# Kernel tuning notes

Measured on AMD Instinct MI355X. Metric: run time of the kernel, lower is better.

## Reference

```python
import jax, jax.numpy as jnp
import numpy as np

V = 32000; D = 256; H = 8; L = 2; FF = 1024; S = 512; B = 32
M = 4096          # mem_max_entries
NC = 10           # num_classes
K = 4             # retrieve top-k
TH = 0.5          # write threshold
EPS = 1e-8


def setup_inputs() -> dict:
    key = jax.random.key(0)
    ks = jax.random.split(key, 24)
    s = 0.02
    def nrm(k, shape):
        return jax.random.normal(k, shape, jnp.float32) * s
    return {
        "input_ids": jax.random.randint(ks[0], (B, S), 0, V),
        "tok_emb": nrm(ks[1], (V, D)),
        "pos_emb": nrm(ks[2], (S, D)),
        # per-layer params stacked on leading dim L
        "Wqkv": nrm(ks[3], (L, 3 * D, D)), "bqkv": jnp.zeros((L, 3 * D)),
        "Wo": nrm(ks[4], (L, D, D)), "bo": jnp.zeros((L, D)),
        "ln1_g": jnp.ones((L, D)), "ln1_b": jnp.zeros((L, D)),
        "W1": nrm(ks[5], (L, FF, D)), "b1": jnp.zeros((L, FF)),
        "W2": nrm(ks[6], (L, D, FF)), "b2": jnp.zeros((L, D)),
        "ln2_g": jnp.ones((L, D)), "ln2_b": jnp.zeros((L, D)),
        # write gate MLP (d -> d -> 1, sigmoid)
        "Wg1": nrm(ks[7], (D, D)), "bg1": jnp.zeros((D,)),
        "Wg2": nrm(ks[8], (1, D)), "bg2": jnp.zeros((1,)),
        # classifier
        "Wc": nrm(ks[9], (NC, D)), "bc": jnp.zeros((NC,)),
    }


def _layer_norm(x, g, b):
    m = x.mean(-1, keepdims=True)
    v = ((x - m) ** 2).mean(-1, keepdims=True)
    return (x - m) / jnp.sqrt(v + 1e-5) * g + b


def _encoder_layer(x, Wqkv, bqkv, Wo, bo, g1, b1, W1, bf1, W2, bf2, g2, b2):
    # post-LN TransformerEncoderLayer, relu activation, batch_first
    Bx, Sx, Dx = x.shape
    dh = Dx // H
    qkv = x @ Wqkv.T + bqkv                     # [B,S,3D]
    q, k, v = jnp.split(qkv, 3, axis=-1)
    def heads(t):
        return t.reshape(Bx, Sx, H, dh).transpose(0, 2, 1, 3)  # [B,H,S,dh]
    q, k, v = heads(q), heads(k), heads(v)
    scores = jnp.einsum("bhqd,bhkd->bhqk", q, k) / jnp.sqrt(jnp.float32(dh))
    attn = jax.nn.softmax(scores, axis=-1)
    o = jnp.einsum("bhqk,bhkd->bhqd", attn, v)
    o = o.transpose(0, 2, 1, 3).reshape(Bx, Sx, Dx)
    o = o @ Wo.T + bo
    x = _layer_norm(x + o, g1, b1)
    ff = jax.nn.relu(x @ W1.T + bf1) @ W2.T + bf2
    return _layer_norm(x + ff, g2, b2)


def reference(input_ids, tok_emb, pos_emb, Wqkv, bqkv, Wo, bo, ln1_g, ln1_b,
              W1, b1, W2, b2, ln2_g, ln2_b, Wg1, bg1, Wg2, bg2, Wc, bc):
    Bx, Sx = input_ids.shape
    x = tok_emb[input_ids] + pos_emb[jnp.arange(Sx)][None, :, :]
    for l in range(L):
        x = _encoder_layer(x, Wqkv[l], bqkv[l], Wo[l], bo[l], ln1_g[l], ln1_b[l],
                           W1[l], b1[l], W2[l], b2[l], ln2_g[l], ln2_b[l])
    h = x                                        # [B,S,D]
    cls_state = h[:, 0, :]                       # [B,D]

    # --- write gate: per-token store into external memory (capped FIFO scatter) ---
    flat_h = h.reshape(-1, D)                    # [B*S, D]
    probs = jax.nn.sigmoid(jax.nn.relu(flat_h @ Wg1.T + bg1) @ Wg2.T + bg2)[:, 0]
    mask = probs > TH                            # [B*S]
    slot = jnp.cumsum(mask.astype(jnp.int32)) - 1
    valid = mask & (slot < M)
    idx = jnp.where(valid, slot, M)              # overflow -> dummy row M
    mem = jnp.zeros((M + 1, D), jnp.float32).at[idx].set(flat_h)[:M]
    count = jnp.minimum(mask.sum(), M)
    occupied = jnp.arange(M) < count             # [M]

    # --- top-k cosine retrieval with CLS as query ---
    qn = cls_state / (jnp.linalg.norm(cls_state, axis=-1, keepdims=True) + EPS)
    kn = mem / (jnp.linalg.norm(mem, axis=-1, keepdims=True) + EPS)
    sims = qn @ kn.T                             # [B,M]
    sims = jnp.where(occupied[None, :], sims, -1e9)
    top_sims, top_idx = jax.lax.top_k(sims, K)   # [B,K]
    vals = mem[top_idx]                          # [B,K,D] (unoccupied rows are zero)
    attn = jax.nn.softmax(top_sims, axis=-1)
    mem_vec = jnp.einsum("bk,bkd->bd", attn, vals)
    mem_vec = jnp.where(count > 0, mem_vec, 0.0)

    cls_aug = cls_state + mem_vec
    return cls_aug @ Wc.T + bc                   # [B,NC]
```

## Files before the change

kernel.cpp:

```cpp
#include <hip/hip_runtime.h>
#include <math.h>

#define D_   256
#define H_   8
#define L_   2
#define FF_  1024
#define S_   512
#define B_   32
#define M_   4096
#define NC_  10
#define ROWS (B_*S_)

typedef __attribute__((ext_vector_type(8))) short bf16x8;
typedef __attribute__((ext_vector_type(4))) float f32x4;
typedef unsigned int uint32;

__device__ __forceinline__ float wave_sum(float v) {
#pragma unroll
  for (int off = 1; off < 64; off <<= 1) v += __shfl_xor(v, off, 64);
  return v;
}

__device__ __forceinline__ unsigned short bf16_rne(float x) {
  unsigned int b = __float_as_uint(x);
  return (unsigned short)((b + 0x7FFFu + ((b >> 16) & 1u)) >> 16);
}
__device__ __forceinline__ float bf16_f(unsigned short h) {
  return __uint_as_float(((unsigned int)h) << 16);
}
__device__ __forceinline__ uint32 pack_split(float x) {
  const unsigned short h = bf16_rne(x);
  const unsigned short l = bf16_rne(x - bf16_f(h));
  return (uint32)h | ((uint32)l << 16);
}
__device__ __forceinline__ void unpack_store(unsigned short* Hq, unsigned short* Lq,
                                             int off, uint4 v) {
  uint2 hp, lp;
  hp.x = (v.x & 0xffffu) | (v.y << 16);
  hp.y = (v.z & 0xffffu) | (v.w << 16);
  lp.x = (v.x >> 16) | (v.y & 0xffff0000u);
  lp.y = (v.z >> 16) | (v.w & 0xffff0000u);
  *(uint2*)&Hq[off] = hp;
  *(uint2*)&Lq[off] = lp;
}
__device__ __forceinline__ bf16x8 ld_frag(const unsigned short* p, int off) {
  union { uint2 u[2]; bf16x8 v; } x;
  x.u[0] = *(const uint2*)(p + off);
  x.u[1] = *(const uint2*)(p + off + 4);
  return x.v;
}

__global__ __launch_bounds__(256) void pack_f32(const float* __restrict__ src,
                                                uint32* __restrict__ dst, int n4) {
  const int i = blockIdx.x * 256 + threadIdx.x;
  if (i < n4) {
    const float4 v = ((const float4*)src)[i];
    uint4 o;
    o.x = pack_split(v.x); o.y = pack_split(v.y);
    o.z = pack_split(v.z); o.w = pack_split(v.w);
    ((uint4*)dst)[i] = o;
  }
}

__global__ __launch_bounds__(256) void emb_kernel(const int* __restrict__ ids,
                                                  const float* __restrict__ tok,
                                                  const float* __restrict__ pos,
                                                  float* __restrict__ x,
                                                  uint32* __restrict__ xp) {
  const int row  = blockIdx.x * 4 + (threadIdx.x >> 6);
  const int lane = threadIdx.x & 63;
  const int id = ids[row];
  const int s  = row & (S_ - 1);
  const float4 t = *(const float4*)(tok + (size_t)id * D_ + lane * 4);
  const float4 p = *(const float4*)(pos + (size_t)s  * D_ + lane * 4);
  float4 r; r.x = t.x + p.x; r.y = t.y + p.y; r.z = t.z + p.z; r.w = t.w + p.w;
  *(float4*)(x + (size_t)row * D_ + lane * 4) = r;
  uint4 o;
  o.x = pack_split(r.x); o.y = pack_split(r.y);
  o.z = pack_split(r.z); o.w = pack_split(r.w);
  *(uint4*)(xp + (size_t)row * D_ + lane * 4) = o;
}

#define LP 36
template<int RELU, int PACKOUT>
__global__ __launch_bounds__(256, 2) void gemm_mfma(const uint32* __restrict__ Ap,
                                                    const uint32* __restrict__ Bp,
                                                    const float* __restrict__ bias,
                                                    float* __restrict__ C,
                                                    uint32* __restrict__ Cp,
                                                    int K, int N, int NX) {
  __shared__ __align__(16) unsigned short Ah[128 * LP];
  __shared__ __align__(16) unsigned short Al[128 * LP];
  __shared__ __align__(16) unsigned short Bh[128 * LP];
  __shared__ __align__(16) unsigned short Bl[128 * LP];

  const int q8 = gridDim.x >> 3;
  const int orig = (blockIdx.x & 7) * q8 + (blockIdx.x >> 3);
  const int by = orig / NX, bx = orig % NX;
  const int m0 = by * 128, n0 = bx * 128;

  const int tid  = threadIdx.x;
  const int lane = tid & 63;
  const int wid  = tid >> 6;
  const int wm = wid >> 1, wn = wid & 1;
  const int lrow  = lane & 15;
  const int khalf = (lane >> 4) * 8;

  const int srow = tid >> 3;
  const int kq   = (tid & 7) << 2;
  const uint32* Aptr = Ap + (size_t)(m0 + srow) * K + kq;
  const uint32* Bptr = Bp + (size_t)(n0 + srow) * K + kq;

  f32x4 acc[4][4];
#pragma unroll
  for (int i = 0; i < 4; i++)
#pragma unroll
    for (int j = 0; j < 4; j++) acc[i][j] = (f32x4){0.f, 0.f, 0.f, 0.f};

  uint4 pa[4], pb[4];
#pragma unroll
  for (int j = 0; j < 4; j++) {
    pa[j] = *(const uint4*)(Aptr + (size_t)j * 32 * K);
    pb[j] = *(const uint4*)(Bptr + (size_t)j * 32 * K);
  }

  for (int k0 = 0; k0 < K; k0 += 32) {
    const int kn = (k0 + 32 < K) ? (k0 + 32) : k0;
    uint4 na[4], nb[4];
#pragma unroll
    for (int j = 0; j < 4; j++) {
      na[j] = *(const uint4*)(Aptr + (size_t)j * 32 * K + kn);
      nb[j] = *(const uint4*)(Bptr + (size_t)j * 32 * K + kn);
    }

    __syncthreads();
#pragma unroll
    for (int j = 0; j < 4; j++) {
      unpack_store(Ah, Al, (srow + j * 32) * LP + kq, pa[j]);
      unpack_store(Bh, Bl, (srow + j * 32) * LP + kq, pb[j]);
    }
    __syncthreads();

    bf16x8 ah[4], al[4], bh[4], bl[4];
#pragma unroll
    for (int f = 0; f < 4; f++) {
      const int rA = (wm * 64 + f * 16 + lrow) * LP + khalf;
      const int rB = (wn * 64 + f * 16 + lrow) * LP + khalf;
      ah[f] = ld_frag(Ah, rA);
      al[f] = ld_frag(Al, rA);
      bh[f] = ld_frag(Bh, rB);
      bl[f] = ld_frag(Bl, rB);
    }
#pragma unroll
    for (int fm = 0; fm < 4; fm++)
#pragma unroll
      for (int fn = 0; fn < 4; fn++) {
        acc[fm][fn] = __builtin_amdgcn_mfma_f32_16x16x32_bf16(ah[fm], bh[fn], acc[fm][fn], 0, 0, 0);
        acc[fm][fn] = __builtin_amdgcn_mfma_f32_16x16x32_bf16(ah[fm], bl[fn], acc[fm][fn], 0, 0, 0);
        acc[fm][fn] = __builtin_amdgcn_mfma_f32_16x16x32_bf16(al[fm], bh[fn], acc[fm][fn], 0, 0, 0);
      }
#pragma unroll
    for (int j = 0; j < 4; j++) { pa[j] = na[j]; pb[j] = nb[j]; }
  }

#pragma unroll
  for (int fm = 0; fm < 4; fm++)
#pragma unroll
    for (int fn = 0; fn < 4; fn++) {
      const int mrow = m0 + wm * 64 + fm * 16 + (lane >> 4) * 4;
      const int ncol = n0 + wn * 64 + fn * 16 + (lane & 15);
      const float bi = bias[ncol];
#pragma unroll
      for (int r = 0; r < 4; r++) {
        float v = acc[fm][fn][r] + bi;
        if (RELU) v = fmaxf(v, 0.f);
        if (PACKOUT) Cp[(size_t)(mrow + r) * N + ncol] = pack_split(v);
        else         C[(size_t)(mrow + r) * N + ncol] = v;
      }
    }
}

template<int MODE>
__global__ __launch_bounds__(512, 2) void gemm_ln(const uint32* __restrict__ Ap,
                                                  const uint32* __restrict__ Bp,
                                                  const float* __restrict__ bias,
                                                  const float* __restrict__ resid,
                                                  const float* __restrict__ g,
                                                  const float* __restrict__ beta,
                                                  const float* __restrict__ Wg2,
                                                  const float* __restrict__ bg2,
                                                  float* __restrict__ outF,
                                                  uint32* __restrict__ outP,
                                                  int* __restrict__ mask,
                                                  int K) {
  __shared__ __align__(16) unsigned short Ah[64 * LP];
  __shared__ __align__(16) unsigned short Al[64 * LP];
  __shared__ __align__(16) unsigned short Bh[256 * LP];
  __shared__ __align__(16) unsigned short Bl[256 * LP];
  __shared__ float psumS[4][64];
  __shared__ float psumQ[4][64];
  __shared__ float meanL[64];
  __shared__ float invL[64];

  const int q8 = gridDim.x >> 3;
  const int m0 = ((blockIdx.x & 7) * q8 + (blockIdx.x >> 3)) * 64;

  const int tid  = threadIdx.x;
  const int lane = tid & 63;
  const int wid  = tid >> 6;
  const int wm = wid >> 2, wn = wid & 3;
  const int lrow  = lane & 15;
  const int khalf = (lane >> 4) * 8;

  const int srow = tid >> 3;
  const int kq   = (tid & 7) << 2;
  const uint32* Aptr = Ap + (size_t)(m0 + srow) * K + kq;
  const uint32* Bptr = Bp + (size_t)srow * K + kq;

  f32x4 acc[2][4];
#pragma unroll
  for (int i = 0; i < 2; i++)
#pragma unroll
    for (int j = 0; j < 4; j++) acc[i][j] = (f32x4){0.f, 0.f, 0.f, 0.f};

  uint4 pa, pb[4];
  pa = *(const uint4*)Aptr;
#pragma unroll
  for (int j = 0; j < 4; j++) pb[j] = *(const uint4*)(Bptr + (size_t)j * 64 * K);

  for (int k0 = 0; k0 < K; k0 += 32) {
    const int kn = (k0 + 32 < K) ? (k0 + 32) : k0;
    uint4 na, nb[4];
    na = *(const uint4*)(Aptr + kn);
#pragma unroll
    for (int j = 0; j < 4; j++) nb[j] = *(const uint4*)(Bptr + (size_t)j * 64 * K + kn);

    __syncthreads();
    unpack_store(Ah, Al, srow * LP + kq, pa);
#pragma unroll
    for (int j = 0; j < 4; j++)
      unpack_store(Bh, Bl, (srow + j * 64) * LP + kq, pb[j]);
    __syncthreads();

    bf16x8 ah[2], al[2], bh[4], bl[4];
#pragma unroll
    for (int fm = 0; fm < 2; fm++) {
      const int r = (wm * 32 + fm * 16 + lrow) * LP + khalf;
      ah[fm] = ld_frag(Ah, r);
      al[fm] = ld_frag(Al, r);
    }
#pragma unroll
    for (int fn = 0; fn < 4; fn++) {
      const int r = (wn * 64 + fn * 16 + lrow) * LP + khalf;
      bh[fn] = ld_frag(Bh, r);
      bl[fn] = ld_frag(Bl, r);
    }
#pragma unroll
    for (int fm = 0; fm < 2; fm++)
#pragma unroll
      for (int fn = 0; fn < 4; fn++) {
        acc[fm][fn] = __builtin_amdgcn_mfma_f32_16x16x32_bf16(ah[fm], bh[fn], acc[fm][fn], 0, 0, 0);
        acc[fm][fn] = __builtin_amdgcn_mfma_f32_16x16x32_bf16(ah[fm], bl[fn], acc[fm][fn], 0, 0, 0);
        acc[fm][fn] = __builtin_amdgcn_mfma_f32_16x16x32_bf16(al[fm], bh[fn], acc[fm][fn], 0, 0, 0);
      }
    pa = na;
#pragma unroll
    for (int j = 0; j < 4; j++) pb[j] = nb[j];
  }

  int cc[4];
  float bi[4];
#pragma unroll
  for (int fn = 0; fn < 4; fn++) {
    cc[fn] = wn * 64 + fn * 16 + (lane & 15);
    bi[fn] = bias[cc[fn]];
  }

  float vv[2][4][4];
  float rs[2][4], rq[2][4];

  if (MODE == 0) {
#pragma unroll
    for (int fm = 0; fm < 2; fm++)
#pragma unroll
      for (int r = 0; r < 4; r++) {
        const int row = m0 + wm * 32 + fm * 16 + (lane >> 4) * 4 + r;
        float s = 0.f, q = 0.f;
#pragma unroll
        for (int fn = 0; fn < 4; fn++) {
          const float a = acc[fm][fn][r] + bi[fn] + resid[(size_t)row * 256 + cc[fn]];
          vv[fm][fn][r] = a;
          s += a; q += a * a;
        }
        rs[fm][r] = s; rq[fm][r] = q;
      }
  } else {
    float wg[4];
#pragma unroll
    for (int fn = 0; fn < 4; fn++) wg[fn] = Wg2[cc[fn]];
#pragma unroll
    for (int fm = 0; fm < 2; fm++)
#pragma unroll
      for (int r = 0; r < 4; r++) {
        float s = 0.f;
#pragma unroll
        for (int fn = 0; fn < 4; fn++)
          s += fmaxf(acc[fm][fn][r] + bi[fn], 0.f) * wg[fn];
        rs[fm][r] = s;
      }
  }

#pragma unroll
  for (int off = 1; off < 16; off <<= 1) {
#pragma unroll
    for (int fm = 0; fm < 2; fm++)
#pragma unroll
      for (int r = 0; r < 4; r++) {
        rs[fm][r] += __shfl_xor(rs[fm][r], off, 64);
        if (MODE == 0) rq[fm][r] += __shfl_xor(rq[fm][r], off, 64);
      }
  }
  if ((lane & 15) == 0) {
#pragma unroll
    for (int fm = 0; fm < 2; fm++)
#pragma unroll
      for (int r = 0; r < 4; r++) {
        const int rloc = wm * 32 + fm * 16 + (lane >> 4) * 4 + r;
        psumS[wn][rloc] = rs[fm][r];
        if (MODE == 0) psumQ[wn][rloc] = rq[fm][r];
      }
  }
  __syncthreads();
  if (tid < 64) {
    float s = 0.f, q = 0.f;
#pragma unroll
    for (int w = 0; w < 4; w++) {
      s += psumS[w][tid];
      if (MODE == 0) q += psumQ[w][tid];
    }
    if (MODE == 0) {
      const float mean = s * (1.f / 256.f);
      const float var = q * (1.f / 256.f) - mean * mean;
      meanL[tid] = mean;
      invL[tid] = rsqrtf(var + 1e-5f);
    } else {
      mask[m0 + tid] = (s + bg2[0]) > 0.f ? 1 : 0;
    }
  }
  if (MODE == 0) {
    __syncthreads();
#pragma unroll
    for (int fm = 0; fm < 2; fm++)
#pragma unroll
      for (int r = 0; r < 4; r++) {
        const int rloc = wm * 32 + fm * 16 + (lane >> 4) * 4 + r;
        const int row = m0 + rloc;
        const float mu = meanL[rloc], iv = invL[rloc];
#pragma unroll
        for (int fn = 0; fn < 4; fn++) {
          const float y = (vv[fm][fn][r] - mu) * iv * g[cc[fn]] + beta[cc[fn]];
          outF[(size_t)row * 256 + cc[fn]] = y;
          outP[(size_t)row * 256 + cc[fn]] = pack_split(y);
        }
      }
  }
}

#define KP 36
#define VP 516
__global__ __launch_bounds__(1024, 4) void attn_mfma(const uint32* __restrict__ qkv,
                                                     uint32* __restrict__ o) {
  __shared__ __align__(16) unsigned short Kh[512 * KP];
  __shared__ __align__(16) unsigned short Kl[512 * KP];
  __shared__ __align__(16) unsigned short Vth[32 * VP];
  __shared__ __align__(16) unsigned short Vtl[32 * VP];

  const int q8g = gridDim.x >> 3;
  const int obh = (blockIdx.x & 7) * q8g + (blockIdx.x >> 3);
  const int b = obh >> 3, h = obh & 7;
  const int tid = threadIdx.x;
  const int lane = tid & 63;
  const int wv = tid >> 6;
  const uint32* base = qkv + (size_t)b * (S_ * 768) + h * 32;

  if (tid < 512) {
    const int slot = tid;
    const int s5 = slot & 31;
    const int orig = (slot & ~31) + 8 * ((s5 >> 2) & 3) + ((s5 >> 4) << 2) + (s5 & 3);
    const uint32* p = base + (size_t)orig * 768 + 256;
#pragma unroll
    for (int j = 0; j < 8; j++)
      unpack_store(Kh, Kl, slot * KP + j * 4, *(const uint4*)(p + j * 4));
  } else {
    const int u  = tid - 512;
    const int kp = u & 255;
    const int dg = (u >> 8) * 16;
    const uint32* p0 = base + (size_t)(2 * kp) * 768 + 512 + dg;
    const uint32* p1 = p0 + 768;
    union { uint4 u4[4]; uint32 w[16]; } a0, a1;
#pragma unroll
    for (int i = 0; i < 4; i++) {
      a0.u4[i] = *(const uint4*)(p0 + i * 4);
      a1.u4[i] = *(const uint4*)(p1 + i * 4);
    }
#pragma unroll
    for (int d = 0; d < 16; d++) {
      const uint32 w0 = a0.w[d], w1 = a1.w[d];
      *(uint32*)&Vth[(dg + d) * VP + 2 * kp] = (w0 & 0xffffu) | (w1 << 16);
      *(uint32*)&Vtl[(dg + d) * VP + 2 * kp] = (w0 >> 16) | (w1 & 0xffff0000u);
    }
  }

  const int q0 = wv * 32;
  bf16x8 qh[2], ql[2];
#pragma unroll
  for (int f = 0; f < 2; f++) {
    const uint32* qp = base + (size_t)(q0 + f * 16 + (lane & 15)) * 768 + ((lane >> 4) * 8);
    union { uint4 u4[2]; uint32 w[8]; } qu;
    qu.u4[0] = *(const uint4*)qp;
    qu.u4[1] = *(const uint4*)(qp + 4);
    bf16x8 vh, vl;
#pragma unroll
    for (int j = 0; j < 8; j++) {
      const uint32 p = qu.w[j];
      const float qf = __uint_as_float(p << 16) + __uint_as_float(p & 0xffff0000u);
      const float sv = qf * 0.17677669529663687f;
      const unsigned short hh = bf16_rne(sv);
      vh[j] = (short)hh;
      vl[j] = (short)bf16_rne(sv - bf16_f(hh));
    }
    qh[f] = vh; ql[f] = vl;
  }

  __syncthreads();

  f32x4 oacc[2][2];
#pragma unroll
  for (int i = 0; i < 2; i++)
#pragma unroll
    for (int j = 0; j < 2; j++) oacc[i][j] = (f32x4){0.f, 0.f, 0.f, 0.f};
  float lacc[2] = {0.f, 0.f};

  for (int kt = 0; kt < S_; kt += 32) {
    bf16x8 kah[2], kal[2];
#pragma unroll
    for (int u = 0; u < 2; u++) {
      const int off = (kt + u * 16 + (lane & 15)) * KP + ((lane >> 4) * 8);
      kah[u] = ld_frag(Kh, off);
      kal[u] = ld_frag(Kl, off);
    }
    bf16x8 vah[2], val[2];
#pragma unroll
    for (int df = 0; df < 2; df++) {
      const int off = (df * 16 + (lane & 15)) * VP + kt + ((lane >> 4) * 8);
      vah[df] = ld_frag(Vth, off);
      val[df] = ld_frag(Vtl, off);
    }
    f32x4 s[2][2];
#pragma unroll
    for (int u = 0; u < 2; u++)
#pragma unroll
      for (int f = 0; f < 2; f++) {
        f32x4 a = (f32x4){0.f, 0.f, 0.f, 0.f};
        a = __builtin_amdgcn_mfma_f32_16x16x32_bf16(kal[u], qh[f], a, 0, 0, 0);
        a = __builtin_amdgcn_mfma_f32_16x16x32_bf16(kah[u], ql[f], a, 0, 0, 0);
        a = __builtin_amdgcn_mfma_f32_16x16x32_bf16(kah[u], qh[f], a, 0, 0, 0);
        s[u][f] = a;
      }
#pragma unroll
    for (int f = 0; f < 2; f++) {
      union { uint32 w[4]; bf16x8 v; } ph, pl;
#pragma unroll
      for (int u = 0; u < 2; u++) {
        const float p0 = __expf(s[u][f][0]);
        const float p1 = __expf(s[u][f][1]);
        const float p2 = __expf(s[u][f][2]);
        const float p3 = __expf(s[u][f][3]);
        lacc[f] += (p0 + p1) + (p2 + p3);
        unsigned int h01, h23;
        asm volatile("v_cvt_pk_bf16_f32 %0, %1, %2" : "=v"(h01) : "v"(p0), "v"(p1));
        asm volatile("v_cvt_pk_bf16_f32 %0, %1, %2" : "=v"(h23) : "v"(p2), "v"(p3));
        const float r0 = p0 - __uint_as_float(h01 << 16);
        const float r1 = p1 - __uint_as_float(h01 & 0xffff0000u);
        const float r2 = p2 - __uint_as_float(h23 << 16);
        const float r3 = p3 - __uint_as_float(h23 & 0xffff0000u);
        unsigned int l01, l23;
        asm volatile("v_cvt_pk_bf16_f32 %0, %1, %2" : "=v"(l01) : "v"(r0), "v"(r1));
        asm volatile("v_cvt_pk_bf16_f32 %0, %1, %2" : "=v"(l23) : "v"(r2), "v"(r3));
        ph.w[u * 2 + 0] = h01;
        ph.w[u * 2 + 1] = h23;
        pl.w[u * 2 + 0] = l01;
        pl.w[u * 2 + 1] = l23;
      }
#pragma unroll
      for (int df = 0; df < 2; df++) {
        oacc[df][f] = __builtin_amdgcn_mfma_f32_16x16x32_bf16(val[df], ph.v, oacc[df][f], 0, 0, 0);
        oacc[df][f] = __builtin_amdgcn_mfma_f32_16x16x32_bf16(vah[df], pl.v, oacc[df][f], 0, 0, 0);
        oacc[df][f] = __builtin_amdgcn_mfma_f32_16x16x32_bf16(vah[df], ph.v, oacc[df][f], 0, 0, 0);
      }
    }
  }

#pragma unroll
  for (int f = 0; f < 2; f++) {
    lacc[f] += __shfl_xor(lacc[f], 16, 64);
    lacc[f] += __shfl_xor(lacc[f], 32, 64);
  }
#pragma unroll
  for (int f = 0; f < 2; f++) {
    const float inv = 1.f / lacc[f];
    const int q = q0 + f * 16 + (lane & 15);
    uint32* op = o + (size_t)(b * S_ + q) * D_ + h * 32;
#pragma unroll
    for (int df = 0; df < 2; df++) {
      const int dbase = df * 16 + (lane >> 4) * 4;
#pragma unroll
      for (int r = 0; r < 4; r++)
        op[dbase + r] = pack_split(oacc[df][f][r] * inv);
    }
  }
}

__global__ __launch_bounds__(256) void scan_kernel(const int* __restrict__ mask,
                                                   int* __restrict__ slots,
                                                   int* __restrict__ countp) {
  __shared__ int wtot[4];
  const int tid = threadIdx.x;
  const int lane = tid & 63, wid = tid >> 6;
  const int base = tid * 64;
  int s = 0;
#pragma unroll 8
  for (int i = 0; i < 64; i++) s += mask[base + i];
  int inc = s;
#pragma unroll
  for (int off = 1; off < 64; off <<= 1) {
    const int t = __shfl_up(inc, off, 64);
    if (lane >= off) inc += t;
  }
  if (lane == 63) wtot[wid] = inc;
  __syncthreads();
  int woff = 0;
#pragma unroll
  for (int w = 0; w < 4; w++) woff += (w < wid) ? wtot[w] : 0;
  const int total = wtot[0] + wtot[1] + wtot[2] + wtot[3];
  if (tid == 0) countp[0] = total < M_ ? total : M_;
  int run = woff + inc - s;
  for (int i = 0; i < 64; i++) {
    const int r = base + i;
    const int mk = mask[r];
    slots[r] = (mk && run < M_) ? run : -1;
    run += mk;
  }
}

__global__ __launch_bounds__(256) void scatter_kernel(const float* __restrict__ h,
                                                      const int* __restrict__ slots,
                                                      float* __restrict__ mem) {
  const int row  = blockIdx.x * 4 + (threadIdx.x >> 6);
  const int lane = threadIdx.x & 63;
  const int sl = slots[row];
  if (sl >= 0)
    *(float4*)(mem + (size_t)sl * D_ + lane * 4) =
        *(const float4*)(h + (size_t)row * D_ + lane * 4);
}

__global__ __launch_bounds__(256) void qnorm_kernel(const float* __restrict__ h,
                                                    float* __restrict__ qden) {
  const int b    = blockIdx.x * 4 + (threadIdx.x >> 6);
  const int lane = threadIdx.x & 63;
  const float4 c = *(const float4*)(h + (size_t)b * S_ * D_ + lane * 4);
  float sq = c.x * c.x + c.y * c.y + c.z * c.z + c.w * c.w;
  sq = wave_sum(sq);
  if (lane == 0) qden[b] = sqrtf(sq) + 1e-8f;
}

__global__ __launch_bounds__(256) void sims_kernel(const float* __restrict__ h,
                                                   const float* __restrict__ mem,
                                                   const float* __restrict__ qden,
                                                   const int* __restrict__ countp,
                                                   float* __restrict__ sims) {
  __shared__ float cls[B_ * D_];
  __shared__ float qd[B_];
  const int tid = threadIdx.x;
  const int lane = tid & 63, wid = tid >> 6;
  for (int i = tid; i < B_ * D_ / 4; i += 256) {
    const int flat = i * 4;
    const int b = flat >> 8, d = flat & 255;
    *(float4*)&cls[flat] = *(const float4*)(h + (size_t)b * S_ * D_ + d);
  }
  if (tid < B_) qd[tid] = qden[tid];
  __syncthreads();
  const int count = countp[0];
  const int r = blockIdx.x * 4 + wid;
  const float4 m4 = *(const float4*)(mem + (size_t)r * D_ + lane * 4);
  float sq = m4.x * m4.x + m4.y * m4.y + m4.z * m4.z + m4.w * m4.w;
  sq = wave_sum(sq);
  const float rn = sqrtf(sq) + 1e-8f;
  if (r < count) {
    for (int b = 0; b < B_; b++) {
      const float4 c4 = *(const float4*)&cls[b * D_ + lane * 4];
      float dt = m4.x * c4.x + m4.y * c4.y + m4.z * c4.z + m4.w * c4.w;
      dt = wave_sum(dt);
      if (lane == 0) sims[b * M_ + r] = dt / (qd[b] * rn);
    }
  } else if (lane == 0) {
    for (int b = 0; b < B_; b++) sims[b * M_ + r] = -1e9f;
  }
}

__global__ __launch_bounds__(256) void topk_mix(const float* __restrict__ h,
                                                const float* __restrict__ mem,
                                                const float* __restrict__ simsg,
                                                const int* __restrict__ countp,
                                                const float* __restrict__ Wc,
                                                const float* __restrict__ bc,
                                                float* __restrict__ out) {
  __shared__ float sims[M_];
  __shared__ float cls[D_];
  __shared__ float wv4[4];
  __shared__ int   wi4[4];
  __shared__ float aug[D_];
  __shared__ float tv[4];
  __shared__ int   tix[4];

  const int b = blockIdx.x, tid = threadIdx.x;
  const int lane = tid & 63, wid = tid >> 6;
  const int count = countp[0];

  for (int i = tid; i < M_; i += 256) sims[i] = simsg[b * M_ + i];
  cls[tid] = h[(size_t)b * S_ * D_ + tid];
  __syncthreads();

  for (int k = 0; k < 4; k++) {
    float bv = -INFINITY; int bi = 1 << 30;
#pragma unroll
    for (int rr = 0; rr < M_ / 256; rr++) {
      const int r = tid + rr * 256;
      const float v = sims[r];
      if (v > bv || (v == bv && r < bi)) { bv = v; bi = r; }
    }
#pragma unroll
    for (int off = 1; off < 64; off <<= 1) {
      const float ov = __shfl_xor(bv, off, 64);
      const int   oi = __shfl_xor(bi, off, 64);
      if (ov > bv || (ov == bv && oi < bi)) { bv = ov; bi = oi; }
    }
    if (lane == 0) { wv4[wid] = bv; wi4[wid] = bi; }
    __syncthreads();
    if (tid == 0) {
      float bb = wv4[0]; int bbi = wi4[0];
#pragma unroll
      for (int i = 1; i < 4; i++)
        if (wv4[i] > bb || (wv4[i] == bb && wi4[i] < bbi)) { bb = wv4[i]; bbi = wi4[i]; }
      tv[k] = bb; tix[k] = bbi; sims[bbi] = -INFINITY;
    }
    __syncthreads();
  }

  float w[4];
  {
    const float mx = tv[0];
    float ws = 0.f;
#pragma unroll
    for (int k = 0; k < 4; k++) { w[k] = expf(tv[k] - mx); ws += w[k]; }
    const float inv = 1.f / ws;
#pragma unroll
    for (int k = 0; k < 4; k++) w[k] *= inv;
  }

  {
    float mv = 0.f;
    if (count > 0) {
#pragma unroll
      for (int k = 0; k < 4; k++) mv = fmaf(w[k], mem[(size_t)tix[k] * D_ + tid], mv);
    }
    aug[tid] = cls[tid] + mv;
  }
  __syncthreads();

  const float4 a4 = *(const float4*)&aug[lane * 4];
  for (int c = wid; c < NC_; c += 4) {
    const float4 wc = *(const float4*)(Wc + (size_t)c * D_ + lane * 4);
    float dt = a4.x * wc.x + a4.y * wc.y + a4.z * wc.z + a4.w * wc.w;
    dt = wave_sum(dt);
    if (lane == 0) out[b * NC_ + c] = dt + bc[c];
  }
}

extern "C" void kernel_launch(void* const* d_in, const int* in_sizes, int n_in,
                              void* d_out, int out_size, void* d_ws, size_t ws_size,
                              hipStream_t stream) {
  const int*   ids  = (const int*)d_in[0];
  const float* tok  = (const float*)d_in[1];
  const float* pos  = (const float*)d_in[2];
  const float* Wqkv = (const float*)d_in[3];
  const float* bqkv = (const float*)d_in[4];
  const float* Wo   = (const float*)d_in[5];
  const float* bo   = (const float*)d_in[6];
  const float* ln1g = (const float*)d_in[7];
  const float* ln1b = (const float*)d_in[8];
  const float* W1   = (const float*)d_in[9];
  const float* b1   = (const float*)d_in[10];
  const float* W2   = (const float*)d_in[11];
  const float* b2   = (const float*)d_in[12];
  const float* ln2g = (const float*)d_in[13];
  const float* ln2b = (const float*)d_in[14];
  const float* Wg1  = (const float*)d_in[15];
  const float* bg1  = (const float*)d_in[16];
  const float* Wg2  = (const float*)d_in[17];
  const float* bg2  = (const float*)d_in[18];
  const float* Wc   = (const float*)d_in[19];
  const float* bc   = (const float*)d_in[20];
  float* out = (float*)d_out;

  float*  xA    = (float*)d_ws;
  float*  xB    = xA  + (size_t)ROWS * D_;
  uint32* xAp   = (uint32*)(xB + (size_t)ROWS * D_);
  uint32* xBp   = xAp + (size_t)ROWS * D_;
  uint32* obp   = xBp + (size_t)ROWS * D_;
  uint32* bigp  = obp + (size_t)ROWS * D_;
  uint32* Wqkvp = bigp + (size_t)ROWS * FF_;
  uint32* Wop   = Wqkvp + (size_t)L_ * 768 * 256;
  uint32* W1p   = Wop   + (size_t)L_ * 256 * 256;
  uint32* W2p   = W1p   + (size_t)L_ * 1024 * 256;
  uint32* Wg1p  = W2p   + (size_t)L_ * 256 * 1024;
  float*  mem   = (float*)(Wg1p + 256 * 256);
  float*  qden  = mem + (size_t)M_ * D_;
  float*  sims  = qden + 64;
  int*    mask  = (int*)(sims + (size_t)B_ * M_);
  int*    slots = mask + ROWS;
  int*    cnt   = slots + ROWS;

  pack_f32<<<(L_ * 768 * 256 / 4 + 255) / 256, 256, 0, stream>>>(Wqkv, Wqkvp, L_ * 768 * 256 / 4);
  pack_f32<<<(L_ * 256 * 256 / 4 + 255) / 256, 256, 0, stream>>>(Wo, Wop, L_ * 256 * 256 / 4);
  pack_f32<<<(L_ * 1024 * 256 / 4 + 255) / 256, 256, 0, stream>>>(W1, W1p, L_ * 1024 * 256 / 4);
  pack_f32<<<(L_ * 256 * 1024 / 4 + 255) / 256, 256, 0, stream>>>(W2, W2p, L_ * 256 * 1024 / 4);
  pack_f32<<<(256 * 256 / 4 + 255) / 256, 256, 0, stream>>>(Wg1, Wg1p, 256 * 256 / 4);

  emb_kernel<<<ROWS / 4, 256, 0, stream>>>(ids, tok, pos, xA, xAp);

  for (int l = 0; l < L_; l++) {
    gemm_mfma<0, 1><<<768, 256, 0, stream>>>(
        xAp, Wqkvp + (size_t)l * 768 * 256, bqkv + l * 768, nullptr, bigp, 256, 768, 6);
    attn_mfma<<<B_ * H_, 1024, 0, stream>>>(bigp, obp);
    gemm_ln<0><<<ROWS / 64, 512, 0, stream>>>(
        obp, Wop + (size_t)l * 256 * 256, bo + l * 256, xA,
        ln1g + l * 256, ln1b + l * 256, nullptr, nullptr, xB, xBp, nullptr, 256);
    gemm_mfma<1, 1><<<1024, 256, 0, stream>>>(
        xBp, W1p + (size_t)l * 1024 * 256, b1 + l * 1024, nullptr, bigp, 256, 1024, 8);
    gemm_ln<0><<<ROWS / 64, 512, 0, stream>>>(
        bigp, W2p + (size_t)l * 256 * 1024, b2 + l * 256, xB,
        ln2g + l * 256, ln2b + l * 256, nullptr, nullptr, xA, xAp, nullptr, 1024);
  }

  gemm_ln<1><<<ROWS / 64, 512, 0, stream>>>(
      xAp, Wg1p, bg1, nullptr, nullptr, nullptr, Wg2, bg2, nullptr, nullptr, mask, 256);
  scan_kernel<<<1, 256, 0, stream>>>(mask, slots, cnt);
  (void)hipMemsetAsync(mem, 0, (size_t)M_ * D_ * sizeof(float), stream);
  scatter_kernel<<<ROWS / 4, 256, 0, stream>>>(xA, slots, mem);

  qnorm_kernel<<<B_ / 4, 256, 0, stream>>>(xA, qden);
  sims_kernel<<<M_ / 4, 256, 0, stream>>>(xA, mem, qden, cnt, sims);
  topk_mix<<<B_, 256, 0, stream>>>(xA, mem, sims, cnt, Wc, bc, out);
}
```

Baseline: 417.6 us.

## Double-buffer LDS in gemm_ln and raise wave priority around MFMA blocks

The gemm_ln kernel now keeps two LDS buffers for the A/B split-bf16 tiles, with a two-stage register prefetch. Each iteration stores the next tile into the other buffer while computing on the current one, leaving one barrier per iteration instead of two. This doubles shared memory use, so launch bounds drop to one block per SM of 512 threads, which lowers occupancy. s_setprio hints are also placed around the MFMA bursts in the plain GEMM, gemm_ln and attention kernels to favour matrix-issuing waves.

After: 436.6 us. +4.6%, slower.

```diff
diff --git a/kernel.cpp b/kernel.cpp
--- a/kernel.cpp
+++ b/kernel.cpp
@@ -151,6 +151,7 @@
       bh[f] = ld_frag(Bh, rB);
       bl[f] = ld_frag(Bl, rB);
     }
+    __builtin_amdgcn_s_setprio(1);
 #pragma unroll
     for (int fm = 0; fm < 4; fm++)
 #pragma unroll
@@ -159,6 +160,7 @@
         acc[fm][fn] = __builtin_amdgcn_mfma_f32_16x16x32_bf16(ah[fm], bl[fn], acc[fm][fn], 0, 0, 0);
         acc[fm][fn] = __builtin_amdgcn_mfma_f32_16x16x32_bf16(al[fm], bh[fn], acc[fm][fn], 0, 0, 0);
       }
+    __builtin_amdgcn_s_setprio(0);
 #pragma unroll
     for (int j = 0; j < 4; j++) { pa[j] = na[j]; pb[j] = nb[j]; }
   }
@@ -181,7 +183,7 @@
 }
 
 template<int MODE>
-__global__ __launch_bounds__(512, 2) void gemm_ln(const uint32* __restrict__ Ap,
+__global__ __launch_bounds__(512, 1) void gemm_ln(const uint32* __restrict__ Ap,
                                                   const uint32* __restrict__ Bp,
                                                   const float* __restrict__ bias,
                                                   const float* __restrict__ resid,
@@ -193,10 +195,10 @@
                                                   uint32* __restrict__ outP,
                                                   int* __restrict__ mask,
                                                   int K) {
-  __shared__ __align__(16) unsigned short Ah[64 * LP];
-  __shared__ __align__(16) unsigned short Al[64 * LP];
-  __shared__ __align__(16) unsigned short Bh[256 * LP];
-  __shared__ __align__(16) unsigned short Bl[256 * LP];
+  __shared__ __align__(16) unsigned short Ah[2][64 * LP];
+  __shared__ __align__(16) unsigned short Al[2][64 * LP];
+  __shared__ __align__(16) unsigned short Bh[2][256 * LP];
+  __shared__ __align__(16) unsigned short Bl[2][256 * LP];
   __shared__ float psumS[4][64];
   __shared__ float psumQ[4][64];
   __shared__ float meanL[64];
@@ -223,38 +225,52 @@
 #pragma unroll
     for (int j = 0; j < 4; j++) acc[i][j] = (f32x4){0.f, 0.f, 0.f, 0.f};
 
-  uint4 pa, pb[4];
-  pa = *(const uint4*)Aptr;
-#pragma unroll
-  for (int j = 0; j < 4; j++) pb[j] = *(const uint4*)(Bptr + (size_t)j * 64 * K);
+  uint4 r1a, r1b[4];
+  {
+    uint4 a0 = *(const uint4*)Aptr;
+    uint4 b0[4];
+#pragma unroll
+    for (int j = 0; j < 4; j++) b0[j] = *(const uint4*)(Bptr + (size_t)j * 64 * K);
+    unpack_store(Ah[0], Al[0], srow * LP + kq, a0);
+#pragma unroll
+    for (int j = 0; j < 4; j++)
+      unpack_store(Bh[0], Bl[0], (srow + j * 64) * LP + kq, b0[j]);
+    const int k1 = (32 < K) ? 32 : 0;
+    r1a = *(const uint4*)(Aptr + k1);
+#pragma unroll
+    for (int j = 0; j < 4; j++) r1b[j] = *(const uint4*)(Bptr + (size_t)j * 64 * K + k1);
+  }
+  __syncthreads();
 
   for (int k0 = 0; k0 < K; k0 += 32) {
-    const int kn = (k0 + 32 < K) ? (k0 + 32) : k0;
-    uint4 na, nb[4];
-    na = *(const uint4*)(Aptr + kn);
-#pragma unroll
-    for (int j = 0; j < 4; j++) nb[j] = *(const uint4*)(Bptr + (size_t)j * 64 * K + kn);
-
-    __syncthreads();
-    unpack_store(Ah, Al, srow * LP + kq, pa);
-#pragma unroll
-    for (int j = 0; j < 4; j++)
-      unpack_store(Bh, Bl, (srow + j * 64) * LP + kq, pb[j]);
-    __syncthreads();
+    const int cur = (k0 >> 5) & 1, nxt = cur ^ 1;
+    const int k2 = (k0 + 64 < K) ? (k0 + 64) : k0;
+    uint4 r2a = *(const uint4*)(Aptr + k2);
+    uint4 r2b[4];
+#pragma unroll
+    for (int j = 0; j < 4; j++) r2b[j] = *(const uint4*)(Bptr + (size_t)j * 64 * K + k2);
+
+    if (k0 + 32 < K) {
+      unpack_store(Ah[nxt], Al[nxt], srow * LP + kq, r1a);
+#pragma unroll
+      for (int j = 0; j < 4; j++)
+        unpack_store(Bh[nxt], Bl[nxt], (srow + j * 64) * LP + kq, r1b[j]);
+    }
 
     bf16x8 ah[2], al[2], bh[4], bl[4];
 #pragma unroll
     for (int fm = 0; fm < 2; fm++) {
       const int r = (wm * 32 + fm * 16 + lrow) * LP + khalf;
-      ah[fm] = ld_frag(Ah, r);
-      al[fm] = ld_frag(Al, r);
+      ah[fm] = ld_frag(Ah[cur], r);
+      al[fm] = ld_frag(Al[cur], r);
     }
 #pragma unroll
     for (int fn = 0; fn < 4; fn++) {
       const int r = (wn * 64 + fn * 16 + lrow) * LP + khalf;
-      bh[fn] = ld_frag(Bh, r);
-      bl[fn] = ld_frag(Bl, r);
-    }
+      bh[fn] = ld_frag(Bh[cur], r);
+      bl[fn] = ld_frag(Bl[cur], r);
+    }
+    __builtin_amdgcn_s_setprio(1);
 #pragma unroll
     for (int fm = 0; fm < 2; fm++)
 #pragma unroll
@@ -263,9 +279,11 @@
         acc[fm][fn] = __builtin_amdgcn_mfma_f32_16x16x32_bf16(ah[fm], bl[fn], acc[fm][fn], 0, 0, 0);
         acc[fm][fn] = __builtin_amdgcn_mfma_f32_16x16x32_bf16(al[fm], bh[fn], acc[fm][fn], 0, 0, 0);
       }
-    pa = na;
-#pragma unroll
-    for (int j = 0; j < 4; j++) pb[j] = nb[j];
+    __builtin_amdgcn_s_setprio(0);
+    __syncthreads();
+    r1a = r2a;
+#pragma unroll
+    for (int j = 0; j < 4; j++) r1b[j] = r2b[j];
   }
 
   int cc[4];
@@ -457,6 +475,7 @@
       val[df] = ld_frag(Vtl, off);
     }
     f32x4 s[2][2];
+    __builtin_amdgcn_s_setprio(1);
 #pragma unroll
     for (int u = 0; u < 2; u++)
 #pragma unroll
@@ -467,6 +486,7 @@
         a = __builtin_amdgcn_mfma_f32_16x16x32_bf16(kah[u], qh[f], a, 0, 0, 0);
         s[u][f] = a;
       }
+    __builtin_amdgcn_s_setprio(0);
 #pragma unroll
     for (int f = 0; f < 2; f++) {
       union { uint32 w[4]; bf16x8 v; } ph, pl;
@@ -492,12 +512,14 @@
         pl.w[u * 2 + 0] = l01;
         pl.w[u * 2 + 1] = l23;
       }
+      __builtin_amdgcn_s_setprio(1);
 #pragma unroll
       for (int df = 0; df < 2; df++) {
         oacc[df][f] = __builtin_amdgcn_mfma_f32_16x16x32_bf16(val[df], ph.v, oacc[df][f], 0, 0, 0);
         oacc[df][f] = __builtin_amdgcn_mfma_f32_16x16x32_bf16(vah[df], pl.v, oacc[df][f], 0, 0, 0);
         oacc[df][f] = __builtin_amdgcn_mfma_f32_16x16x32_bf16(vah[df], ph.v, oacc[df][f], 0, 0, 0);
       }
+      __builtin_amdgcn_s_setprio(0);
     }
   }
 
```

## Double-buffer K/V tiles in attention kernel to overlap staging with MFMA

Applied to the files above, without the earlier changes.

The attention kernel used to stage all 512 keys and values for a (batch, head) into shared memory before computing. It now splits them into four 128-key tiles held in two shared-memory buffers, loading the next tile while the current one is processed and syncing once per tile. This cuts shared memory per block and aims to hide global-load latency behind the MFMA work. The launch-bounds occupancy hint drops from 4 to 2, and the extra barriers may offset the gain.

After: 427.8 us. +2.4%, slower.

```diff
diff --git a/kernel.cpp b/kernel.cpp
--- a/kernel.cpp
+++ b/kernel.cpp
@@ -366,14 +366,14 @@
   }
 }
 
-#define KP 36
-#define VP 516
-__global__ __launch_bounds__(1024, 4) void attn_mfma(const uint32* __restrict__ qkv,
+#define KP  36
+#define VPt 132
+__global__ __launch_bounds__(1024, 2) void attn_mfma(const uint32* __restrict__ qkv,
                                                      uint32* __restrict__ o) {
-  __shared__ __align__(16) unsigned short Kh[512 * KP];
-  __shared__ __align__(16) unsigned short Kl[512 * KP];
-  __shared__ __align__(16) unsigned short Vth[32 * VP];
-  __shared__ __align__(16) unsigned short Vtl[32 * VP];
+  __shared__ __align__(16) unsigned short Kh[2][128 * KP];
+  __shared__ __align__(16) unsigned short Kl[2][128 * KP];
+  __shared__ __align__(16) unsigned short Vth[2][32 * VPt];
+  __shared__ __align__(16) unsigned short Vtl[2][32 * VPt];
 
   const int q8g = gridDim.x >> 3;
   const int obh = (blockIdx.x & 7) * q8g + (blockIdx.x >> 3);
@@ -383,33 +383,32 @@
   const int wv = tid >> 6;
   const uint32* base = qkv + (size_t)b * (S_ * 768) + h * 32;
 
-  if (tid < 512) {
-    const int slot = tid;
-    const int s5 = slot & 31;
-    const int orig = (slot & ~31) + 8 * ((s5 >> 2) & 3) + ((s5 >> 4) << 2) + (s5 & 3);
-    const uint32* p = base + (size_t)orig * 768 + 256;
-#pragma unroll
-    for (int j = 0; j < 8; j++)
-      unpack_store(Kh, Kl, slot * KP + j * 4, *(const uint4*)(p + j * 4));
-  } else {
-    const int u  = tid - 512;
-    const int kp = u & 255;
-    const int dg = (u >> 8) * 16;
-    const uint32* p0 = base + (size_t)(2 * kp) * 768 + 512 + dg;
-    const uint32* p1 = p0 + 768;
-    union { uint4 u4[4]; uint32 w[16]; } a0, a1;
-#pragma unroll
-    for (int i = 0; i < 4; i++) {
-      a0.u4[i] = *(const uint4*)(p0 + i * 4);
-      a1.u4[i] = *(const uint4*)(p1 + i * 4);
-    }
-#pragma unroll
-    for (int d = 0; d < 16; d++) {
-      const uint32 w0 = a0.w[d], w1 = a1.w[d];
-      *(uint32*)&Vth[(dg + d) * VP + 2 * kp] = (w0 & 0xffffu) | (w1 << 16);
-      *(uint32*)&Vtl[(dg + d) * VP + 2 * kp] = (w0 >> 16) | (w1 & 0xffff0000u);
-    }
-  }
+  auto stage = [&](int t, int bf) {
+    if (tid < 512) {
+      const int sl = tid >> 2, part = tid & 3;
+      const int s5 = sl & 31;
+      const int orig = (sl & ~31) + 8 * ((s5 >> 2) & 3) + ((s5 >> 4) << 2) + (s5 & 3);
+      const uint32* p = base + (size_t)(t * 128 + orig) * 768 + 256;
+      const int j0 = part * 2;
+      unpack_store(Kh[bf], Kl[bf], sl * KP + (j0 + 0) * 4, *(const uint4*)(p + (j0 + 0) * 4));
+      unpack_store(Kh[bf], Kl[bf], sl * KP + (j0 + 1) * 4, *(const uint4*)(p + (j0 + 1) * 4));
+    } else {
+      const int u  = tid - 512;
+      const int kp = u & 63;
+      const int dq = u >> 6;
+      const uint32* p0 = base + (size_t)(t * 128 + 2 * kp) * 768 + 512 + dq * 4;
+      const uint32* p1 = p0 + 768;
+      union { uint4 u4; uint32 w[4]; } a0, a1;
+      a0.u4 = *(const uint4*)p0;
+      a1.u4 = *(const uint4*)p1;
+#pragma unroll
+      for (int d = 0; d < 4; d++) {
+        const uint32 w0 = a0.w[d], w1 = a1.w[d];
+        *(uint32*)&Vth[bf][(dq * 4 + d) * VPt + 2 * kp] = (w0 & 0xffffu) | (w1 << 16);
+        *(uint32*)&Vtl[bf][(dq * 4 + d) * VPt + 2 * kp] = (w0 >> 16) | (w1 & 0xffff0000u);
+      }
+    }
+  };
 
   const int q0 = wv * 32;
   bf16x8 qh[2], ql[2];
@@ -432,6 +431,7 @@
     qh[f] = vh; ql[f] = vl;
   }
 
+  stage(0, 0);
   __syncthreads();
 
   f32x4 oacc[2][2];
@@ -441,64 +441,70 @@
     for (int j = 0; j < 2; j++) oacc[i][j] = (f32x4){0.f, 0.f, 0.f, 0.f};
   float lacc[2] = {0.f, 0.f};
 
-  for (int kt = 0; kt < S_; kt += 32) {
-    bf16x8 kah[2], kal[2];
-#pragma unroll
-    for (int u = 0; u < 2; u++) {
-      const int off = (kt + u * 16 + (lane & 15)) * KP + ((lane >> 4) * 8);
-      kah[u] = ld_frag(Kh, off);
-      kal[u] = ld_frag(Kl, off);
-    }
-    bf16x8 vah[2], val[2];
-#pragma unroll
-    for (int df = 0; df < 2; df++) {
-      const int off = (df * 16 + (lane & 15)) * VP + kt + ((lane >> 4) * 8);
-      vah[df] = ld_frag(Vth, off);
-      val[df] = ld_frag(Vtl, off);
-    }
-    f32x4 s[2][2];
-#pragma unroll
-    for (int u = 0; u < 2; u++)
+  for (int t = 0; t < 4; t++) {
+    const int cur = t & 1;
+    if (t + 1 < 4) stage(t + 1, cur ^ 1);
+
+    for (int kt = 0; kt < 128; kt += 32) {
+      bf16x8 kah[2], kal[2];
+#pragma unroll
+      for (int u = 0; u < 2; u++) {
+        const int off = (kt + u * 16 + (lane & 15)) * KP + ((lane >> 4) * 8);
+        kah[u] = ld_frag(Kh[cur], off);
+        kal[u] = ld_frag(Kl[cur], off);
+      }
+      bf16x8 vah[2], val[2];
+#pragma unroll
+      for (int df = 0; df < 2; df++) {
+        const int off = (df * 16 + (lane & 15)) * VPt + kt + ((lane >> 4) * 8);
+        vah[df] = ld_frag(Vth[cur], off);
+        val[df] = ld_frag(Vtl[cur], off);
+      }
+      f32x4 s[2][2];
+#pragma unroll
+      for (int u = 0; u < 2; u++)
+#pragma unroll
+        for (int f = 0; f < 2; f++) {
+          f32x4 a = (f32x4){0.f, 0.f, 0.f, 0.f};
+          a = __builtin_amdgcn_mfma_f32_16x16x32_bf16(kal[u], qh[f], a, 0, 0, 0);
+          a = __builtin_amdgcn_mfma_f32_16x16x32_bf16(kah[u], ql[f], a, 0, 0, 0);
+          a = __builtin_amdgcn_mfma_f32_16x16x32_bf16(kah[u], qh[f], a, 0, 0, 0);
+          s[u][f] = a;
+        }
 #pragma unroll
       for (int f = 0; f < 2; f++) {
-        f32x4 a = (f32x4){0.f, 0.f, 0.f, 0.f};
-        a = __builtin_amdgcn_mfma_f32_16x16x32_bf16(kal[u], qh[f], a, 0, 0, 0);
-        a = __builtin_amdgcn_mfma_f32_16x16x32_bf16(kah[u], ql[f], a, 0, 0, 0);
-        a = __builtin_amdgcn_mfma_f32_16x16x32_bf16(kah[u], qh[f], a, 0, 0, 0);
-        s[u][f] = a;
-      }
-#pragma unroll
-    for (int f = 0; f < 2; f++) {
-      union { uint32 w[4]; bf16x8 v; } ph, pl;
-#pragma unroll
-      for (int u = 0; u < 2; u++) {
-        const float p0 = __expf(s[u][f][0]);
-        const float p1 = __expf(s[u][f][1]);
-        const float p2 = __expf(s[u][f][2]);
-        const float p3 = __expf(s[u][f][3]);
-        lacc[f] += (p0 + p1) + (p2 + p3);
-        unsigned int h01, h23;
-        asm volatile("v_cvt_pk_bf16_f32 %0, %1, %2" : "=v"(h01) : "v"(p0), "v"(p1));
-        asm volatile("v_cvt_pk_bf16_f32 %0, %1, %2" : "=v"(h23) : "v"(p2), "v"(p3));
-        const float r0 = p0 - __uint_as_float(h01 << 16);
-        const float r1 = p1 - __uint_as_float(h01 & 0xffff0000u);
-        const float r2 = p2 - __uint_as_float(h23 << 16);
-        const float r3 = p3 - __uint_as_float(h23 & 0xffff0000u);
-        unsigned int l01, l23;
-        asm volatile("v_cvt_pk_bf16_f32 %0, %1, %2" : "=v"(l01) : "v"(r0), "v"(r1));
-        asm volatile("v_cvt_pk_bf16_f32 %0, %1, %2" : "=v"(l23) : "v"(r2), "v"(r3));
-        ph.w[u * 2 + 0] = h01;
-        ph.w[u * 2 + 1] = h23;
-        pl.w[u * 2 + 0] = l01;
-        pl.w[u * 2 + 1] = l23;
-      }
-#pragma unroll
-      for (int df = 0; df < 2; df++) {
-        oacc[df][f] = __builtin_amdgcn_mfma_f32_16x16x32_bf16(val[df], ph.v, oacc[df][f], 0, 0, 0);
-        oacc[df][f] = __builtin_amdgcn_mfma_f32_16x16x32_bf16(vah[df], pl.v, oacc[df][f], 0, 0, 0);
-        oacc[df][f] = __builtin_amdgcn_mfma_f32_16x16x32_bf16(vah[df], ph.v, oacc[df][f], 0, 0, 0);
-      }
-    }
+        union { uint32 w[4]; bf16x8 v; } ph, pl;
+#pragma unroll
+        for (int u = 0; u < 2; u++) {
+          const float p0 = __expf(s[u][f][0]);
+          const float p1 = __expf(s[u][f][1]);
+          const float p2 = __expf(s[u][f][2]);
+          const float p3 = __expf(s[u][f][3]);
+          lacc[f] += (p0 + p1) + (p2 + p3);
+          unsigned int h01, h23;
+          asm volatile("v_cvt_pk_bf16_f32 %0, %1, %2" : "=v"(h01) : "v"(p0), "v"(p1));
+          asm volatile("v_cvt_pk_bf16_f32 %0, %1, %2" : "=v"(h23) : "v"(p2), "v"(p3));
+          const float r0 = p0 - __uint_as_float(h01 << 16);
+          const float r1 = p1 - __uint_as_float(h01 & 0xffff0000u);
+          const float r2 = p2 - __uint_as_float(h23 << 16);
+          const float r3 = p3 - __uint_as_float(h23 & 0xffff0000u);
+          unsigned int l01, l23;
+          asm volatile("v_cvt_pk_bf16_f32 %0, %1, %2" : "=v"(l01) : "v"(r0), "v"(r1));
+          asm volatile("v_cvt_pk_bf16_f32 %0, %1, %2" : "=v"(l23) : "v"(r2), "v"(r3));
+          ph.w[u * 2 + 0] = h01;
+          ph.w[u * 2 + 1] = h23;
+          pl.w[u * 2 + 0] = l01;
+          pl.w[u * 2 + 1] = l23;
+        }
+#pragma unroll
+        for (int df = 0; df < 2; df++) {
+          oacc[df][f] = __builtin_amdgcn_mfma_f32_16x16x32_bf16(val[df], ph.v, oacc[df][f], 0, 0, 0);
+          oacc[df][f] = __builtin_amdgcn_mfma_f32_16x16x32_bf16(vah[df], pl.v, oacc[df][f], 0, 0, 0);
+          oacc[df][f] = __builtin_amdgcn_mfma_f32_16x16x32_bf16(vah[df], ph.v, oacc[df][f], 0, 0, 0);
+        }
+      }
+    }
+    __syncthreads();
   }
 
 #pragma unroll
```
